# Kernel tuning notes

Hardware: AMD Instinct MI355X
Metric: run time of the kernel (lower is better)

The kernel has to match this reference:

```python
import jax, jax.numpy as jnp
import numpy as np

N_NODES = 100000
N_EDGES = 1600000
NUM_PROP = 5
CAT_PROP = 3
INPUT_DIM = 128
HIDDEN = 128
NUM_REL = 2


def setup_inputs() -> dict:
    key = jax.random.key(0)
    ks = jax.random.split(key, 20)
    s = 0.05
    inp = {
        "x": jax.random.normal(ks[0], (N_NODES, NUM_PROP + CAT_PROP), jnp.float32),
        "edge_index": jax.random.randint(ks[1], (2, N_EDGES), 0, N_NODES, jnp.int64 if jax.config.jax_enable_x64 else jnp.int32),
        "edge_type": jax.random.randint(ks[2], (N_EDGES,), 0, NUM_REL, jnp.int32),
        # numeric / categorical encoders -> input_dim/2 each
        "W_num": jax.random.normal(ks[3], (NUM_PROP, INPUT_DIM // 2), jnp.float32) * s,
        "b_num": jnp.zeros((INPUT_DIM // 2,), jnp.float32),
        "W_cat": jax.random.normal(ks[4], (CAT_PROP, INPUT_DIM // 2), jnp.float32) * s,
        "b_cat": jnp.zeros((INPUT_DIM // 2,), jnp.float32),
        # input projection + PReLU
        "W_in": jax.random.normal(ks[5], (INPUT_DIM, HIDDEN), jnp.float32) * s,
        "b_in": jnp.zeros((HIDDEN,), jnp.float32),
        "prelu_a": jnp.full((HIDDEN,), 0.25, jnp.float32),
        # RGCN layer 1
        "W_rel1": jax.random.normal(ks[6], (NUM_REL, HIDDEN, HIDDEN), jnp.float32) * s,
        "W_root1": jax.random.normal(ks[7], (HIDDEN, HIDDEN), jnp.float32) * s,
        "b_rgcn1": jnp.zeros((HIDDEN,), jnp.float32),
        # RGCN layer 2
        "W_rel2": jax.random.normal(ks[8], (NUM_REL, HIDDEN, HIDDEN), jnp.float32) * s,
        "W_root2": jax.random.normal(ks[9], (HIDDEN, HIDDEN), jnp.float32) * s,
        "b_rgcn2": jnp.zeros((HIDDEN,), jnp.float32),
        # classifier (single Linear)
        "W_cls": jax.random.normal(ks[10], (HIDDEN, HIDDEN), jnp.float32) * s,
        "b_cls": jnp.zeros((HIDDEN,), jnp.float32),
    }
    return inp


def _leaky_relu(x, slope=0.01):
    return jnp.where(x >= 0, x, slope * x)


def _prelu(x, a):
    return jnp.where(x >= 0, x, a * x)


def _rgcn_conv(x, edge_index, edge_type, W_rel, W_root, bias):
    # PyG RGCNConv: out[i] = x[i] @ W_root + bias + sum_r mean_{j in N_r(i)} x[j] @ W_r
    # Aggregate-then-transform (linearity) to avoid per-edge (E, d) @ W products.
    src, dst = edge_index[0], edge_index[1]
    n = x.shape[0]
    x_src = x[src]  # (E, d) gather
    out = x @ W_root + bias
    for r in range(W_rel.shape[0]):
        w = (edge_type == r).astype(x.dtype)  # (E,)
        agg = jax.ops.segment_sum(x_src * w[:, None], dst, num_segments=n)  # (N, d)
        deg = jax.ops.segment_sum(w, dst, num_segments=n)  # (N,)
        out = out + (agg / jnp.clip(deg, 1.0)[:, None]) @ W_rel[r]
    return out


def reference(x, edge_index, edge_type, W_num, b_num, W_cat, b_cat, W_in, b_in,
              prelu_a, W_rel1, W_root1, b_rgcn1, W_rel2, W_root2, b_rgcn2,
              W_cls, b_cls):
    num_prop = x[:, :NUM_PROP]
    cat_prop = x[:, NUM_PROP:NUM_PROP + CAT_PROP]
    n = _leaky_relu(num_prop @ W_num + b_num)
    c = _leaky_relu(cat_prop @ W_cat + b_cat)
    h = jnp.concatenate([n, c], axis=1)
    h = _prelu(h @ W_in + b_in, prelu_a)
    h = _rgcn_conv(h, edge_index, edge_type, W_rel1, W_root1, b_rgcn1)
    # dropout is identity in eval mode
    h = _rgcn_conv(h, edge_index, edge_type, W_rel2, W_root2, b_rgcn2)
    return h @ W_cls + b_cls
```

## Files before the change

### kernel.cpp

```cpp
#include <hip/hip_runtime.h>
#include <cstdint>


typedef short bf16x8 __attribute__((ext_vector_type(8)));
typedef float f32x4  __attribute__((ext_vector_type(4)));

__device__ __forceinline__ unsigned short f2bf(float f) {
    unsigned int u = __builtin_bit_cast(unsigned int, f);
    u += 0x7fff + ((u >> 16) & 1);
    return (unsigned short)(u >> 16);
}
__device__ __forceinline__ float bf2f(unsigned short h) {
    unsigned int u = ((unsigned int)h) << 16;
    return __builtin_bit_cast(float, u);
}
__device__ __forceinline__ float lo16f(unsigned int u) {
    return __builtin_bit_cast(float, u << 16);
}
__device__ __forceinline__ float hi16f(unsigned int u) {
    return __builtin_bit_cast(float, u & 0xffff0000u);
}

__device__ __forceinline__ void gload_lds16(const void* g, void* l) {
    __builtin_amdgcn_global_load_lds(
        (const __attribute__((address_space(1))) void*)g,
        (__attribute__((address_space(3))) void*)l, 16, 0, 0);
}

__global__ __launch_bounds__(256) void k_egemm(
    const float* __restrict__ x,
    const float* __restrict__ Wnum, const float* __restrict__ bnum,
    const float* __restrict__ Wcat, const float* __restrict__ bcat,
    const unsigned short* __restrict__ Bhi, const unsigned short* __restrict__ Blo,
    const float* __restrict__ bias, const float* __restrict__ prelu,
    unsigned short* __restrict__ C_hi, unsigned short* __restrict__ C_lo, int M)
{
    __shared__ unsigned short lds[2][32 * 512];
    const int t = threadIdx.x;
    const int w = t >> 6, lane = t & 63;
    const int laneL = lane & 15, laneH = lane >> 4;
    const int wi = w >> 1, wj = w & 1;
    const int m0 = blockIdx.x * 128;
    const int Mm1 = M - 1;

    f32x4 acc[4][4];
    #pragma unroll
    for (int a = 0; a < 4; ++a)
        #pragma unroll
        for (int b = 0; b < 4; ++b)
            acc[a][b] = (f32x4){0.f, 0.f, 0.f, 0.f};

    auto stage = [&](int s, unsigned short* buf) {
        int koff = s * 32;
        int k8 = koff + laneH * 8;
        #pragma unroll
        for (int c = 0; c < 2; ++c) {
            int j = w + c * 4;
            int rc = j * 16 + laneL;
            int row = (m0 + rc <= Mm1) ? (m0 + rc) : Mm1;
            const float4* xr = (const float4*)(x + (size_t)row * 8);
            float4 X0 = xr[0], X1 = xr[1];
            float a[8];
            if (k8 < 64) {
                const float4* bp = (const float4*)(bnum + k8);
                float4 b0 = bp[0], b1 = bp[1];
                a[0]=b0.x; a[1]=b0.y; a[2]=b0.z; a[3]=b0.w;
                a[4]=b1.x; a[5]=b1.y; a[6]=b1.z; a[7]=b1.w;
                float xs0 = X0.x, xs1 = X0.y, xs2 = X0.z, xs3 = X0.w, xs4 = X1.x;
                const float* wb = Wnum + k8;
                #pragma unroll
                for (int p = 0; p < 5; ++p) {
                    float xp = p==0?xs0 : p==1?xs1 : p==2?xs2 : p==3?xs3 : xs4;
                    const float4* wp = (const float4*)(wb + p * 64);
                    float4 w0 = wp[0], w1 = wp[1];
                    a[0]+=xp*w0.x; a[1]+=xp*w0.y; a[2]+=xp*w0.z; a[3]+=xp*w0.w;
                    a[4]+=xp*w1.x; a[5]+=xp*w1.y; a[6]+=xp*w1.z; a[7]+=xp*w1.w;
                }
            } else {
                int kk = k8 - 64;
                const float4* bp = (const float4*)(bcat + kk);
                float4 b0 = bp[0], b1 = bp[1];
                a[0]=b0.x; a[1]=b0.y; a[2]=b0.z; a[3]=b0.w;
                a[4]=b1.x; a[5]=b1.y; a[6]=b1.z; a[7]=b1.w;
                float xs0 = X1.y, xs1 = X1.z, xs2 = X1.w;
                const float* wb = Wcat + kk;
                #pragma unroll
                for (int p = 0; p < 3; ++p) {
                    float xp = p==0?xs0 : p==1?xs1 : xs2;
                    const float4* wp = (const float4*)(wb + p * 64);
                    float4 w0 = wp[0], w1 = wp[1];
                    a[0]+=xp*w0.x; a[1]+=xp*w0.y; a[2]+=xp*w0.z; a[3]+=xp*w0.w;
                    a[4]+=xp*w1.x; a[5]+=xp*w1.y; a[6]+=xp*w1.z; a[7]+=xp*w1.w;
                }
            }
            unsigned hw[4], lw[4];
            #pragma unroll
            for (int q = 0; q < 4; ++q) {
                float v0 = a[2*q]   >= 0.f ? a[2*q]   : 0.01f * a[2*q];
                float v1 = a[2*q+1] >= 0.f ? a[2*q+1] : 0.01f * a[2*q+1];
                unsigned short h0 = f2bf(v0), h1 = f2bf(v1);
                unsigned short l0 = f2bf(v0 - bf2f(h0)), l1 = f2bf(v1 - bf2f(h1));
                hw[q] = (unsigned)h0 | ((unsigned)h1 << 16);
                lw[q] = (unsigned)l0 | ((unsigned)l1 << 16);
            }
            uint4 ho, lo_;
            ho.x=hw[0]; ho.y=hw[1]; ho.z=hw[2]; ho.w=hw[3];
            lo_.x=lw[0]; lo_.y=lw[1]; lo_.z=lw[2]; lo_.w=lw[3];
            *(uint4*)&buf[(0 * 8 + j) * 512 + lane * 8] = ho;
            *(uint4*)&buf[(1 * 8 + j) * 512 + lane * 8] = lo_;
        }
        #pragma unroll
        for (int c = 4; c < 8; ++c) {
            int chunk = w + c * 4;
            int slot = chunk >> 3, j = chunk & 7;
            const unsigned short* plane = (slot == 2) ? Bhi : Blo;
            int rc = j * 16 + laneL;
            const unsigned short* gp = plane + (size_t)rc * 128 + koff + laneH * 8;
            gload_lds16(gp, &buf[(slot * 8 + j) * 512]);
        }
    };

    stage(0, lds[0]);
    for (int s = 0; s < 4; ++s) {
        unsigned short* cur = lds[s & 1];
        unsigned short* nxt = lds[(s & 1) ^ 1];
        __syncthreads();
        if (s + 1 < 4) stage(s + 1, nxt);
        const bf16x8* fr = (const bf16x8*)cur;
        bf16x8 ah[4], al[4], bh[4], bl[4];
        #pragma unroll
        for (int mi = 0; mi < 4; ++mi) {
            ah[mi] = fr[(0 + wi * 4 + mi) * 64 + lane];
            al[mi] = fr[(8 + wi * 4 + mi) * 64 + lane];
        }
        #pragma unroll
        for (int nj = 0; nj < 4; ++nj) {
            bh[nj] = fr[(16 + wj * 4 + nj) * 64 + lane];
            bl[nj] = fr[(24 + wj * 4 + nj) * 64 + lane];
        }
        #pragma unroll
        for (int mi = 0; mi < 4; ++mi)
            #pragma unroll
            for (int nj = 0; nj < 4; ++nj) {
                acc[mi][nj] = __builtin_amdgcn_mfma_f32_16x16x32_bf16(
                    ah[mi], bh[nj], acc[mi][nj], 0, 0, 0);
                acc[mi][nj] = __builtin_amdgcn_mfma_f32_16x16x32_bf16(
                    ah[mi], bl[nj], acc[mi][nj], 0, 0, 0);
                acc[mi][nj] = __builtin_amdgcn_mfma_f32_16x16x32_bf16(
                    al[mi], bh[nj], acc[mi][nj], 0, 0, 0);
            }
    }

    float bv[4], av[4];
    #pragma unroll
    for (int nj = 0; nj < 4; ++nj) {
        int col = wj * 64 + nj * 16 + laneL;
        bv[nj] = bias[col];
        av[nj] = prelu[col];
    }
    unsigned short* lp = &lds[0][0];
    __syncthreads();
    #pragma unroll
    for (int nj = 0; nj < 4; ++nj) {
        int col = wj * 64 + nj * 16 + laneL;
        #pragma unroll
        for (int mi = 0; mi < 4; ++mi)
            #pragma unroll
            for (int r = 0; r < 4; ++r) {
                int row = wi * 64 + mi * 16 + laneH * 4 + r;
                float v = acc[mi][nj][r] + bv[nj];
                v = v >= 0.f ? v : av[nj] * v;
                lp[row * 128 + col] = f2bf(v);
            }
    }
    __syncthreads();
    {
        const uint4* lsrc = (const uint4*)lp;
        #pragma unroll
        for (int it = 0; it < 8; ++it) {
            int idx = it * 256 + t;
            int row = idx >> 4, c = idx & 15;
            int m = m0 + row;
            if (m < M)
                ((uint4*)(C_hi + (size_t)m * 128))[c] = lsrc[idx];
        }
    }
    __syncthreads();
    #pragma unroll
    for (int nj = 0; nj < 4; ++nj) {
        int col = wj * 64 + nj * 16 + laneL;
        #pragma unroll
        for (int mi = 0; mi < 4; ++mi)
            #pragma unroll
            for (int r = 0; r < 4; ++r) {
                int row = wi * 64 + mi * 16 + laneH * 4 + r;
                float v = acc[mi][nj][r] + bv[nj];
                v = v >= 0.f ? v : av[nj] * v;
                unsigned short h = f2bf(v);
                lp[row * 128 + col] = f2bf(v - bf2f(h));
            }
    }
    __syncthreads();
    {
        const uint4* lsrc = (const uint4*)lp;
        #pragma unroll
        for (int it = 0; it < 8; ++it) {
            int idx = it * 256 + t;
            int row = idx >> 4, c = idx & 15;
            int m = m0 + row;
            if (m < M)
                ((uint4*)(C_lo + (size_t)m * 128))[c] = lsrc[idx];
        }
    }
}

__global__ __launch_bounds__(256) void k_hist(
    const int* __restrict__ ei, const int* __restrict__ et,
    int* __restrict__ cntmatT, int E, int N, int NBINS)
{
    __shared__ int hist[1024];
    const int t = threadIdx.x, blk = blockIdx.x;
    for (int i = t; i < NBINS; i += 256) hist[i] = 0;
    __syncthreads();
    #pragma unroll
    for (int j = 0; j < 8; ++j) {
        int e = blk * 2048 + j * 256 + t;
        if (e < E) atomicAdd(&hist[(et[e] * N + ei[E + e]) >> 8], 1);
    }
    __syncthreads();
    for (int i = t; i < NBINS; i += 256)
        cntmatT[(size_t)blk * NBINS + i] = hist[i];
}

__global__ __launch_bounds__(256) void k_transpose(
    const int* __restrict__ src, int* __restrict__ dst, int R, int C)
{
    __shared__ int tile[32][33];
    int ctiles = (C + 31) >> 5;
    int bx = blockIdx.x % ctiles;
    int by = blockIdx.x / ctiles;
    int tc = threadIdx.x & 31, tr = threadIdx.x >> 5;
    int c0 = bx * 32, r0 = by * 32;
    #pragma unroll
    for (int i = 0; i < 32; i += 8) {
        int r = r0 + tr + i, c = c0 + tc;
        if (r < R && c < C) tile[tr + i][tc] = src[(size_t)r * C + c];
    }
    __syncthreads();
    #pragma unroll
    for (int i = 0; i < 32; i += 8) {
        int r = r0 + tc;
        int c = c0 + tr + i;
        if (r < R && c < C) dst[(size_t)c * R + r] = tile[tc][tr + i];
    }
}

struct WArgs {
    const float* W[8];
    unsigned short* hi[8];
    unsigned short* lo[8];
};
__global__ __launch_bounds__(256) void k_wsplit(WArgs a)
{
    int part = blockIdx.y;
    int idx = blockIdx.x * 256 + threadIdx.x;
    int n = idx >> 7, k = idx & 127;
    float v = a.W[part][(size_t)k * 128 + n];
    unsigned short h = f2bf(v);
    a.hi[part][(size_t)n * 128 + k] = h;
    a.lo[part][(size_t)n * 128 + k] = f2bf(v - bf2f(h));
}

__global__ __launch_bounds__(256) void k_scan1(
    const int* __restrict__ src, int* __restrict__ dst,
    int* __restrict__ bsum, int n)
{
    __shared__ int s[256];
    int t = threadIdx.x;
    int i = blockIdx.x * 256 + t;
    int v = (i < n) ? src[i] : 0;
    s[t] = v;
    __syncthreads();
    #pragma unroll
    for (int d = 1; d < 256; d <<= 1) {
        int add = (t >= d) ? s[t - d] : 0;
        __syncthreads();
        s[t] += add;
        __syncthreads();
    }
    if (i < n) dst[i] = s[t] - v;
    if (t == 255) bsum[blockIdx.x] = s[255];
}

__global__ __launch_bounds__(1024) void k_scan2(int* __restrict__ bsum, int nb)
{
    __shared__ int s[1024];
    int t = threadIdx.x;
    int carry = 0;
    for (int base = 0; base < nb; base += 1024) {
        int i = base + t;
        int v = (i < nb) ? bsum[i] : 0;
        s[t] = v;
        __syncthreads();
        #pragma unroll
        for (int d = 1; d < 1024; d <<= 1) {
            int add = (t >= d) ? s[t - d] : 0;
            __syncthreads();
            s[t] += add;
            __syncthreads();
        }
        if (i < nb) bsum[i] = carry + s[t] - v;
        carry += s[1023];
        __syncthreads();
    }
}

__global__ __launch_bounds__(256) void k_scan3(
    int* __restrict__ dst, const int* __restrict__ bsum, int n)
{
    int i = blockIdx.x * 256 + threadIdx.x;
    if (i < n) dst[i] += bsum[blockIdx.x];
}

__global__ __launch_bounds__(256) void k_binscatter(
    const int* __restrict__ ei, const int* __restrict__ et,
    const int* __restrict__ cntscanT, int* __restrict__ ebuf,
    int E, int N, int NBINS)
{
    __shared__ int base[1024];
    const int t = threadIdx.x;
    const int blk = blockIdx.x;
    for (int i = t; i < NBINS; i += 256)
        base[i] = cntscanT[(size_t)blk * NBINS + i];
    __syncthreads();
    #pragma unroll
    for (int j = 0; j < 8; ++j) {
        int e = blk * 2048 + j * 256 + t;
        if (e < E) {
            unsigned src = (unsigned)ei[e];
            int seg = et[e] * N + ei[E + e];
            int pos = atomicAdd(&base[seg >> 8], 1);
            ebuf[pos] = (int)(((unsigned)(seg & 255) << 24) | src);
        }
    }
}

__global__ __launch_bounds__(256) void k_bincsr(
    const int* __restrict__ cntscan, const int* __restrict__ ebuf,
    int* __restrict__ deg, int* __restrict__ off, int* __restrict__ esrc,
    int E, int nseg, int NBLK, int NBINS)
{
    __shared__ int cnt[256];
    __shared__ int pfx[256];
    __shared__ int cur[256];
    const int b = blockIdx.x;
    const int t = threadIdx.x;
    const int est = cntscan[(size_t)b * NBLK];
    const int een = (b + 1 < NBINS) ? cntscan[(size_t)(b + 1) * NBLK] : E;
    cnt[t] = 0;
    __syncthreads();
    for (int e = est + t; e < een; e += 256)
        atomicAdd(&cnt[((unsigned)ebuf[e]) >> 24], 1);
    __syncthreads();
    int v = cnt[t];
    pfx[t] = v;
    __syncthreads();
    #pragma unroll
    for (int d = 1; d < 256; d <<= 1) {
        int add = (t >= d) ? pfx[t - d] : 0;
        __syncthreads();
        pfx[t] += add;
        __syncthreads();
    }
    int o = est + pfx[t] - v;
    int seg = b * 256 + t;
    if (seg < nseg) { deg[seg] = v; off[seg] = o; }
    cur[t] = o;
    __syncthreads();
    for (int e = est + t; e < een; e += 256) {
        unsigned u = (unsigned)ebuf[e];
        int p = atomicAdd(&cur[u >> 24], 1);
        esrc[p] = (int)(u & 0xffffffu);
    }
}

__global__ __launch_bounds__(256) void k_gather(
    const unsigned short* __restrict__ h_hi,
    const int* __restrict__ esrc,
    const int* __restrict__ off, const int* __restrict__ deg,
    unsigned short* __restrict__ a_hi, int nseg)
{
    int i = blockIdx.x * 8 + (threadIdx.x >> 5);
    if (i >= nseg) return;
    int l32 = threadIdx.x & 31;
    int q = l32 >> 4;
    int l16 = l32 & 15;
    int cnt = deg[i], st = off[i];
    const uint4* hp = (const uint4*)h_hi;
    float a0 = 0.f, a1 = 0.f, a2 = 0.f, a3 = 0.f;
    float a4 = 0.f, a5 = 0.f, a6 = 0.f, a7 = 0.f;
    int e = q;
    for (; e + 6 < cnt; e += 8) {
        int i0 = esrc[st + e + 0];
        int i1 = esrc[st + e + 2];
        int i2 = esrc[st + e + 4];
        int i3 = esrc[st + e + 6];
        uint4 u0 = hp[(size_t)i0 * 16 + l16];
        uint4 u1 = hp[(size_t)i1 * 16 + l16];
        uint4 u2 = hp[(size_t)i2 * 16 + l16];
        uint4 u3 = hp[(size_t)i3 * 16 + l16];
        a0 += lo16f(u0.x); a1 += hi16f(u0.x); a2 += lo16f(u0.y); a3 += hi16f(u0.y);
        a4 += lo16f(u0.z); a5 += hi16f(u0.z); a6 += lo16f(u0.w); a7 += hi16f(u0.w);
        a0 += lo16f(u1.x); a1 += hi16f(u1.x); a2 += lo16f(u1.y); a3 += hi16f(u1.y);
        a4 += lo16f(u1.z); a5 += hi16f(u1.z); a6 += lo16f(u1.w); a7 += hi16f(u1.w);
        a0 += lo16f(u2.x); a1 += hi16f(u2.x); a2 += lo16f(u2.y); a3 += hi16f(u2.y);
        a4 += lo16f(u2.z); a5 += hi16f(u2.z); a6 += lo16f(u2.w); a7 += hi16f(u2.w);
        a0 += lo16f(u3.x); a1 += hi16f(u3.x); a2 += lo16f(u3.y); a3 += hi16f(u3.y);
        a4 += lo16f(u3.z); a5 += hi16f(u3.z); a6 += lo16f(u3.w); a7 += hi16f(u3.w);
    }
    for (; e < cnt; e += 2) {
        uint4 u = hp[(size_t)esrc[st + e] * 16 + l16];
        a0 += lo16f(u.x); a1 += hi16f(u.x); a2 += lo16f(u.y); a3 += hi16f(u.y);
        a4 += lo16f(u.z); a5 += hi16f(u.z); a6 += lo16f(u.w); a7 += hi16f(u.w);
    }
    a0 += __shfl_xor(a0, 16, 64);
    a1 += __shfl_xor(a1, 16, 64);
    a2 += __shfl_xor(a2, 16, 64);
    a3 += __shfl_xor(a3, 16, 64);
    a4 += __shfl_xor(a4, 16, 64);
    a5 += __shfl_xor(a5, 16, 64);
    a6 += __shfl_xor(a6, 16, 64);
    a7 += __shfl_xor(a7, 16, 64);
    if (q == 0) {
        float inv = 1.0f / (float)(cnt > 1 ? cnt : 1);
        uint4 o;
        o.x = (unsigned int)f2bf(a0 * inv) | ((unsigned int)f2bf(a1 * inv) << 16);
        o.y = (unsigned int)f2bf(a2 * inv) | ((unsigned int)f2bf(a3 * inv) << 16);
        o.z = (unsigned int)f2bf(a4 * inv) | ((unsigned int)f2bf(a5 * inv) << 16);
        o.w = (unsigned int)f2bf(a6 * inv) | ((unsigned int)f2bf(a7 * inv) << 16);
        ((uint4*)a_hi)[(size_t)i * 16 + l16] = o;
    }
}

struct GArgs {
    const unsigned short* A_hi[3];
    const unsigned short* A_lo[3];
    const unsigned short* B_hi[3];
    const unsigned short* B_lo[3];
    int alo[3];
    int blo[3];
    const float* bias;
    const float* prelu;
    float* Cf;
    unsigned short* C_hi;
    unsigned short* C_lo;
    int M;
    int P;
};

__global__ __launch_bounds__(256) void k_mgemm(GArgs g)
{
    __shared__ unsigned short lds[2][32 * 512];
    const int t = threadIdx.x;
    const int w = t >> 6, lane = t & 63;
    const int laneL = lane & 15, laneH = lane >> 4;
    const int wi = w >> 1, wj = w & 1;
    const int m0 = blockIdx.x * 128;
    const int Mm1 = g.M - 1;
    const int S = g.P * 4;

    f32x4 acc[4][4];
    #pragma unroll
    for (int a = 0; a < 4; ++a)
        #pragma unroll
        for (int b = 0; b < 4; ++b)
            acc[a][b] = (f32x4){0.f, 0.f, 0.f, 0.f};

    auto stage = [&](int s, unsigned short* buf) {
        int p = s >> 2, koff = (s & 3) * 32;
        const unsigned short* tp[4];
        tp[0] = g.A_hi[p];
        tp[1] = g.alo[p] ? g.A_lo[p] : nullptr;
        tp[2] = g.B_hi[p];
        tp[3] = g.blo[p] ? g.B_lo[p] : nullptr;
        #pragma unroll
        for (int c = 0; c < 8; ++c) {
            int chunk = w + c * 4;
            int slot = chunk >> 3, j = chunk & 7;
            const unsigned short* plane = tp[slot];
            if (!plane) continue;
            int rc = j * 16 + laneL;
            int row = (slot < 2) ? (m0 + rc <= Mm1 ? m0 + rc : Mm1) : rc;
            const unsigned short* gp = plane + (size_t)row * 128 + koff + laneH * 8;
            gload_lds16(gp, &buf[(slot * 8 + j) * 512]);
        }
    };

    stage(0, lds[0]);
    for (int s = 0; s < S; ++s) {
        unsigned short* cur = lds[s & 1];
        unsigned short* nxt = lds[(s & 1) ^ 1];
        __syncthreads();
        if (s + 1 < S) stage(s + 1, nxt);
        int p = s >> 2;
        const bool hasAlo = g.alo[p] != 0;
        const bool hasBlo = g.blo[p] != 0;
        const bf16x8* fr = (const bf16x8*)cur;
        bf16x8 ah[4], al[4], bh[4], bl[4];
        #pragma unroll
        for (int mi = 0; mi < 4; ++mi)
            ah[mi] = fr[(0 + wi * 4 + mi) * 64 + lane];
        if (hasAlo) {
            #pragma unroll
            for (int mi = 0; mi < 4; ++mi)
                al[mi] = fr[(8 + wi * 4 + mi) * 64 + lane];
        }
        #pragma unroll
        for (int nj = 0; nj < 4; ++nj)
            bh[nj] = fr[(16 + wj * 4 + nj) * 64 + lane];
        if (hasBlo) {
            #pragma unroll
            for (int nj = 0; nj < 4; ++nj)
                bl[nj] = fr[(24 + wj * 4 + nj) * 64 + lane];
        }
        #pragma unroll
        for (int mi = 0; mi < 4; ++mi)
            #pragma unroll
            for (int nj = 0; nj < 4; ++nj) {
                acc[mi][nj] = __builtin_amdgcn_mfma_f32_16x16x32_bf16(
                    ah[mi], bh[nj], acc[mi][nj], 0, 0, 0);
                if (hasBlo)
                    acc[mi][nj] = __builtin_amdgcn_mfma_f32_16x16x32_bf16(
                        ah[mi], bl[nj], acc[mi][nj], 0, 0, 0);
                if (hasAlo)
                    acc[mi][nj] = __builtin_amdgcn_mfma_f32_16x16x32_bf16(
                        al[mi], bh[nj], acc[mi][nj], 0, 0, 0);
            }
    }

    const bool hasPrelu = (g.prelu != nullptr);
    float bv[4], av[4];
    #pragma unroll
    for (int nj = 0; nj < 4; ++nj) {
        int col = wj * 64 + nj * 16 + laneL;
        bv[nj] = g.bias[col];
        av[nj] = hasPrelu ? g.prelu[col] : 0.f;
    }

    if (g.Cf) {
        float* lf = (float*)&lds[0][0];
        __syncthreads();
        #pragma unroll
        for (int nj = 0; nj < 4; ++nj) {
            int col = wj * 64 + nj * 16 + laneL;
            #pragma unroll
            for (int mi = 0; mi < 4; ++mi)
                #pragma unroll
                for (int r = 0; r < 4; ++r) {
                    int row = wi * 64 + mi * 16 + laneH * 4 + r;
                    float v = acc[mi][nj][r] + bv[nj];
                    lf[row * 128 + col] = v;
                }
        }
        __syncthreads();
        const uint4* lsrc = (const uint4*)lf;
        #pragma unroll
        for (int it = 0; it < 16; ++it) {
            int idx = it * 256 + t;
            int row = idx >> 5, c = idx & 31;
            int m = m0 + row;
            if (m < g.M)
                ((uint4*)(g.Cf + (size_t)m * 128))[c] = lsrc[idx];
        }
    } else {
        unsigned short* lp = &lds[0][0];
        __syncthreads();
        #pragma unroll
        for (int nj = 0; nj < 4; ++nj) {
            int col = wj * 64 + nj * 16 + laneL;
            #pragma unroll
            for (int mi = 0; mi < 4; ++mi)
                #pragma unroll
                for (int r = 0; r < 4; ++r) {
                    int row = wi * 64 + mi * 16 + laneH * 4 + r;
                    float v = acc[mi][nj][r] + bv[nj];
                    if (hasPrelu) v = v >= 0.f ? v : av[nj] * v;
                    lp[row * 128 + col] = f2bf(v);
                }
        }
        __syncthreads();
        {
            const uint4* lsrc = (const uint4*)lp;
            #pragma unroll
            for (int it = 0; it < 8; ++it) {
                int idx = it * 256 + t;
                int row = idx >> 4, c = idx & 15;
                int m = m0 + row;
                if (m < g.M)
                    ((uint4*)(g.C_hi + (size_t)m * 128))[c] = lsrc[idx];
            }
        }
        __syncthreads();
        #pragma unroll
        for (int nj = 0; nj < 4; ++nj) {
            int col = wj * 64 + nj * 16 + laneL;
            #pragma unroll
            for (int mi = 0; mi < 4; ++mi)
                #pragma unroll
                for (int r = 0; r < 4; ++r) {
                    int row = wi * 64 + mi * 16 + laneH * 4 + r;
                    float v = acc[mi][nj][r] + bv[nj];
                    if (hasPrelu) v = v >= 0.f ? v : av[nj] * v;
                    unsigned short h = f2bf(v);
                    lp[row * 128 + col] = f2bf(v - bf2f(h));
                }
        }
        __syncthreads();
        {
            const uint4* lsrc = (const uint4*)lp;
            #pragma unroll
            for (int it = 0; it < 8; ++it) {
                int idx = it * 256 + t;
                int row = idx >> 4, c = idx & 15;
                int m = m0 + row;
                if (m < g.M)
                    ((uint4*)(g.C_lo + (size_t)m * 128))[c] = lsrc[idx];
            }
        }
    }
}

extern "C" void kernel_launch(void* const* d_in, const int* in_sizes, int n_in,
                              void* d_out, int out_size, void* d_ws, size_t ws_size,
                              hipStream_t stream) {
    const float* x      = (const float*)d_in[0];
    const int*   ei     = (const int*)d_in[1];
    const int*   et     = (const int*)d_in[2];
    const float* Wnum   = (const float*)d_in[3];
    const float* bnum   = (const float*)d_in[4];
    const float* Wcat   = (const float*)d_in[5];
    const float* bcat   = (const float*)d_in[6];
    const float* Win    = (const float*)d_in[7];
    const float* bin    = (const float*)d_in[8];
    const float* pa     = (const float*)d_in[9];
    const float* Wrel1  = (const float*)d_in[10];
    const float* Wroot1 = (const float*)d_in[11];
    const float* brg1   = (const float*)d_in[12];
    const float* Wrel2  = (const float*)d_in[13];
    const float* Wroot2 = (const float*)d_in[14];
    const float* brg2   = (const float*)d_in[15];
    const float* Wcls   = (const float*)d_in[16];
    const float* bcls   = (const float*)d_in[17];
    float* out = (float*)d_out;

    const int N = in_sizes[0] / 8;
    const int E = in_sizes[1] / 2;
    const int nseg = 2 * N;
    const size_t NH = (size_t)N * 128;

    const int NBLK  = (E + 2047) / 2048;
    const int NBINS = (nseg + 255) / 256;
    const long long L = (long long)NBINS * NBLK;

    char* w = (char*)d_ws;
    unsigned short* h0_hi = (unsigned short*)w;  w += NH * 2;
    unsigned short* h0_lo = (unsigned short*)w;  w += NH * 2;
    unsigned short* agg_hi = (unsigned short*)w; w += 2 * NH * 2;
    int* deg      = (int*)w;  w += (size_t)nseg * 4;
    int* off      = (int*)w;  w += (size_t)nseg * 4;
    int* cntmatT  = (int*)w;  w += (size_t)L * 4;
    int* cntmat   = (int*)w;  w += (size_t)L * 4;
    int* cntscan  = (int*)w;  w += (size_t)L * 4;
    int* cntscanT = (int*)w;  w += (size_t)L * 4;
    int* esrc     = (int*)w;  w += (size_t)E * 4;
    int* bsum     = (int*)w;  w += 4096 * 4;
    unsigned short* wplanes = (unsigned short*)w;  w += 8 * 2 * 16384 * 2;

    unsigned short* h1_hi = (unsigned short*)d_out;
    unsigned short* h1_lo = h1_hi + NH;
    unsigned short* h2_hi = h0_hi;
    unsigned short* h2_lo = h0_lo;
    int* ebuf = (int*)d_out;

    unsigned short* whi[8];
    unsigned short* wlo[8];
    for (int i = 0; i < 8; ++i) {
        whi[i] = wplanes + (size_t)i * 2 * 16384;
        wlo[i] = whi[i] + 16384;
    }

    {
        WArgs a;
        a.W[0] = Win;   a.W[1] = Wroot1; a.W[2] = Wrel1; a.W[3] = Wrel1 + 16384;
        a.W[4] = Wroot2; a.W[5] = Wrel2; a.W[6] = Wrel2 + 16384; a.W[7] = Wcls;
        for (int i = 0; i < 8; ++i) { a.hi[i] = whi[i]; a.lo[i] = wlo[i]; }
        k_wsplit<<<dim3(64, 8), 256, 0, stream>>>(a);
    }

    const int gm = (N + 127) / 128;
    const int gg = (nseg + 7) / 8;

    k_hist<<<NBLK, 256, 0, stream>>>(ei, et, cntmatT, E, N, NBINS);

    const int rt = (NBLK + 31) / 32, ct = (NBINS + 31) / 32;
    k_transpose<<<rt * ct, 256, 0, stream>>>(cntmatT, cntmat, NBLK, NBINS);

    const int nb1 = (int)((L + 255) / 256);
    k_scan1<<<nb1, 256, 0, stream>>>(cntmat, cntscan, bsum, (int)L);
    k_scan2<<<1, 1024, 0, stream>>>(bsum, nb1);
    k_scan3<<<nb1, 256, 0, stream>>>(cntscan, bsum, (int)L);

    k_transpose<<<ct * rt, 256, 0, stream>>>(cntscan, cntscanT, NBINS, NBLK);

    k_binscatter<<<NBLK, 256, 0, stream>>>(ei, et, cntscanT, ebuf, E, N, NBINS);
    k_bincsr<<<NBINS, 256, 0, stream>>>(cntscan, ebuf, deg, off, esrc, E, nseg, NBLK, NBINS);

    k_egemm<<<gm, 256, 0, stream>>>(x, Wnum, bnum, Wcat, bcat,
                                    whi[0], wlo[0], bin, pa,
                                    h0_hi, h0_lo, N);

    k_gather<<<gg, 256, 0, stream>>>(h0_hi, esrc, off, deg, agg_hi, nseg);
    {
        GArgs g = {};
        g.A_hi[0] = h0_hi;       g.A_lo[0] = h0_lo;  g.alo[0] = 1; g.blo[0] = 1;
        g.A_hi[1] = agg_hi;      g.alo[1] = 0;       g.blo[1] = 0;
        g.A_hi[2] = agg_hi + NH; g.alo[2] = 0;       g.blo[2] = 0;
        g.B_hi[0] = whi[1]; g.B_lo[0] = wlo[1];
        g.B_hi[1] = whi[2]; g.B_lo[1] = wlo[2];
        g.B_hi[2] = whi[3]; g.B_lo[2] = wlo[3];
        g.bias = brg1; g.prelu = nullptr;
        g.Cf = nullptr; g.C_hi = h1_hi; g.C_lo = h1_lo;
        g.M = N; g.P = 3;
        k_mgemm<<<gm, 256, 0, stream>>>(g);
    }
    k_gather<<<gg, 256, 0, stream>>>(h1_hi, esrc, off, deg, agg_hi, nseg);
    {
        GArgs g = {};
        g.A_hi[0] = h1_hi;       g.A_lo[0] = h1_lo;  g.alo[0] = 1; g.blo[0] = 1;
        g.A_hi[1] = agg_hi;      g.alo[1] = 0;       g.blo[1] = 0;
        g.A_hi[2] = agg_hi + NH; g.alo[2] = 0;       g.blo[2] = 0;
        g.B_hi[0] = whi[4]; g.B_lo[0] = wlo[4];
        g.B_hi[1] = whi[5]; g.B_lo[1] = wlo[5];
        g.B_hi[2] = whi[6]; g.B_lo[2] = wlo[6];
        g.bias = brg2; g.prelu = nullptr;
        g.Cf = nullptr; g.C_hi = h2_hi; g.C_lo = h2_lo;
        g.M = N; g.P = 3;
        k_mgemm<<<gm, 256, 0, stream>>>(g);
    }
    {
        GArgs g = {};
        g.A_hi[0] = h2_hi; g.A_lo[0] = h2_lo; g.alo[0] = 1; g.blo[0] = 1;
        g.B_hi[0] = whi[7]; g.B_lo[0] = wlo[7];
        g.bias = bcls; g.prelu = nullptr;
        g.Cf = out; g.C_hi = nullptr; g.C_lo = nullptr;
        g.M = N; g.P = 1;
        k_mgemm<<<gm, 256, 0, stream>>>(g);
    }
}
```

Baseline: 474.7 us.

## Fuse classifier GEMM into RGCN layer-2 epilogue and merge preprocessing kernels

The classifier linear layer now runs inside the second RGCN GEMM's epilogue. The layer-2 output is split into bf16 hi/lo planes in swizzled LDS and multiplied by the classifier weights there, so the h2 round trip and a separate launch go away. The weight-split and histogram kernels are merged into one launch. The scan-add step is folded into the transpose and into bincsr, and the edge blocks per histogram/scatter block double to 4096. The hi/lo epilogue stores both planes in one pass instead of two. This cuts launches and memory traffic, at the cost of more registers and LDS pressure in the fused epilogue.

```diff
diff --git a/kernel.cpp b/kernel.cpp
--- a/kernel.cpp
+++ b/kernel.cpp
@@ -158,33 +158,8 @@
         bv[nj] = bias[col];
         av[nj] = prelu[col];
     }
-    unsigned short* lp = &lds[0][0];
-    __syncthreads();
-    #pragma unroll
-    for (int nj = 0; nj < 4; ++nj) {
-        int col = wj * 64 + nj * 16 + laneL;
-        #pragma unroll
-        for (int mi = 0; mi < 4; ++mi)
-            #pragma unroll
-            for (int r = 0; r < 4; ++r) {
-                int row = wi * 64 + mi * 16 + laneH * 4 + r;
-                float v = acc[mi][nj][r] + bv[nj];
-                v = v >= 0.f ? v : av[nj] * v;
-                lp[row * 128 + col] = f2bf(v);
-            }
-    }
-    __syncthreads();
-    {
-        const uint4* lsrc = (const uint4*)lp;
-        #pragma unroll
-        for (int it = 0; it < 8; ++it) {
-            int idx = it * 256 + t;
-            int row = idx >> 4, c = idx & 15;
-            int m = m0 + row;
-            if (m < M)
-                ((uint4*)(C_hi + (size_t)m * 128))[c] = lsrc[idx];
-        }
-    }
+    unsigned short* lph = &lds[0][0];
+    unsigned short* lpl = &lds[1][0];
     __syncthreads();
     #pragma unroll
     for (int nj = 0; nj < 4; ++nj) {
@@ -197,39 +172,64 @@
                 float v = acc[mi][nj][r] + bv[nj];
                 v = v >= 0.f ? v : av[nj] * v;
                 unsigned short h = f2bf(v);
-                lp[row * 128 + col] = f2bf(v - bf2f(h));
+                lph[row * 128 + col] = h;
+                lpl[row * 128 + col] = f2bf(v - bf2f(h));
             }
     }
     __syncthreads();
     {
-        const uint4* lsrc = (const uint4*)lp;
+        const uint4* sh = (const uint4*)lph;
+        const uint4* sl = (const uint4*)lpl;
         #pragma unroll
         for (int it = 0; it < 8; ++it) {
             int idx = it * 256 + t;
             int row = idx >> 4, c = idx & 15;
             int m = m0 + row;
-            if (m < M)
-                ((uint4*)(C_lo + (size_t)m * 128))[c] = lsrc[idx];
-        }
-    }
-}
-
-__global__ __launch_bounds__(256) void k_hist(
-    const int* __restrict__ ei, const int* __restrict__ et,
-    int* __restrict__ cntmatT, int E, int N, int NBINS)
+            if (m < M) {
+                ((uint4*)(C_hi + (size_t)m * 128))[c] = sh[idx];
+                ((uint4*)(C_lo + (size_t)m * 128))[c] = sl[idx];
+            }
+        }
+    }
+}
+
+struct WHArgs {
+    const float* W[8];
+    unsigned short* hi[8];
+    unsigned short* lo[8];
+    const int* ei;
+    const int* et;
+    int* cntmatT;
+    int E;
+    int N;
+    int NBINS;
+};
+__global__ __launch_bounds__(256) void k_wsplit_hist(WHArgs a)
 {
     __shared__ int hist[1024];
-    const int t = threadIdx.x, blk = blockIdx.x;
-    for (int i = t; i < NBINS; i += 256) hist[i] = 0;
-    __syncthreads();
-    #pragma unroll
-    for (int j = 0; j < 8; ++j) {
-        int e = blk * 2048 + j * 256 + t;
-        if (e < E) atomicAdd(&hist[(et[e] * N + ei[E + e]) >> 8], 1);
-    }
-    __syncthreads();
-    for (int i = t; i < NBINS; i += 256)
-        cntmatT[(size_t)blk * NBINS + i] = hist[i];
+    const int t = threadIdx.x;
+    const int b = blockIdx.x;
+    if (b < 512) {
+        int part = b >> 6;
+        int idx = (b & 63) * 256 + t;
+        int n = idx >> 7, k = idx & 127;
+        float v = a.W[part][(size_t)k * 128 + n];
+        unsigned short h = f2bf(v);
+        a.hi[part][(size_t)n * 128 + k] = h;
+        a.lo[part][(size_t)n * 128 + k] = f2bf(v - bf2f(h));
+        return;
+    }
+    const int blk = b - 512;
+    for (int i = t; i < a.NBINS; i += 256) hist[i] = 0;
+    __syncthreads();
+    #pragma unroll
+    for (int j = 0; j < 16; ++j) {
+        int e = blk * 4096 + j * 256 + t;
+        if (e < a.E) atomicAdd(&hist[(a.et[e] * a.N + a.ei[a.E + e]) >> 8], 1);
+    }
+    __syncthreads();
+    for (int i = t; i < a.NBINS; i += 256)
+        a.cntmatT[(size_t)blk * a.NBINS + i] = hist[i];
 }
 
 __global__ __launch_bounds__(256) void k_transpose(
@@ -255,20 +255,31 @@
     }
 }
 
-struct WArgs {
-    const float* W[8];
-    unsigned short* hi[8];
-    unsigned short* lo[8];
-};
-__global__ __launch_bounds__(256) void k_wsplit(WArgs a)
-{
-    int part = blockIdx.y;
-    int idx = blockIdx.x * 256 + threadIdx.x;
-    int n = idx >> 7, k = idx & 127;
-    float v = a.W[part][(size_t)k * 128 + n];
-    unsigned short h = f2bf(v);
-    a.hi[part][(size_t)n * 128 + k] = h;
-    a.lo[part][(size_t)n * 128 + k] = f2bf(v - bf2f(h));
+__global__ __launch_bounds__(256) void k_transpose_add(
+    const int* __restrict__ src, int* __restrict__ dst,
+    const int* __restrict__ bsum, int R, int C)
+{
+    __shared__ int tile[32][33];
+    int ctiles = (C + 31) >> 5;
+    int bx = blockIdx.x % ctiles;
+    int by = blockIdx.x / ctiles;
+    int tc = threadIdx.x & 31, tr = threadIdx.x >> 5;
+    int c0 = bx * 32, r0 = by * 32;
+    #pragma unroll
+    for (int i = 0; i < 32; i += 8) {
+        int r = r0 + tr + i, c = c0 + tc;
+        if (r < R && c < C) {
+            size_t idx = (size_t)r * C + c;
+            tile[tr + i][tc] = src[idx] + bsum[idx >> 8];
+        }
+    }
+    __syncthreads();
+    #pragma unroll
+    for (int i = 0; i < 32; i += 8) {
+        int r = r0 + tc;
+        int c = c0 + tr + i;
+        if (r < R && c < C) dst[(size_t)c * R + r] = tile[tc][tr + i];
+    }
 }
 
 __global__ __launch_bounds__(256) void k_scan1(
@@ -315,13 +326,6 @@
     }
 }
 
-__global__ __launch_bounds__(256) void k_scan3(
-    int* __restrict__ dst, const int* __restrict__ bsum, int n)
-{
-    int i = blockIdx.x * 256 + threadIdx.x;
-    if (i < n) dst[i] += bsum[blockIdx.x];
-}
-
 __global__ __launch_bounds__(256) void k_binscatter(
     const int* __restrict__ ei, const int* __restrict__ et,
     const int* __restrict__ cntscanT, int* __restrict__ ebuf,
@@ -334,8 +338,8 @@
         base[i] = cntscanT[(size_t)blk * NBINS + i];
     __syncthreads();
     #pragma unroll
-    for (int j = 0; j < 8; ++j) {
-        int e = blk * 2048 + j * 256 + t;
+    for (int j = 0; j < 16; ++j) {
+        int e = blk * 4096 + j * 256 + t;
         if (e < E) {
             unsigned src = (unsigned)ei[e];
             int seg = et[e] * N + ei[E + e];
@@ -346,7 +350,8 @@
 }
 
 __global__ __launch_bounds__(256) void k_bincsr(
-    const int* __restrict__ cntscan, const int* __restrict__ ebuf,
+    const int* __restrict__ cntscan, const int* __restrict__ bsum,
+    const int* __restrict__ ebuf,
     int* __restrict__ deg, int* __restrict__ off, int* __restrict__ esrc,
     int E, int nseg, int NBLK, int NBINS)
 {
@@ -355,8 +360,13 @@
     __shared__ int cur[256];
     const int b = blockIdx.x;
     const int t = threadIdx.x;
-    const int est = cntscan[(size_t)b * NBLK];
-    const int een = (b + 1 < NBINS) ? cntscan[(size_t)(b + 1) * NBLK] : E;
+    size_t i0 = (size_t)b * NBLK;
+    const int est = cntscan[i0] + bsum[i0 >> 8];
+    int een = E;
+    if (b + 1 < NBINS) {
+        size_t i1 = (size_t)(b + 1) * NBLK;
+        een = cntscan[i1] + bsum[i1 >> 8];
+    }
     cnt[t] = 0;
     __syncthreads();
     for (int e = est + t; e < een; e += 256)
@@ -451,11 +461,14 @@
     int blo[3];
     const float* bias;
     const float* prelu;
-    float* Cf;
     unsigned short* C_hi;
     unsigned short* C_lo;
     int M;
     int P;
+    const unsigned short* clsBhi;
+    const unsigned short* clsBlo;
+    const float* clsBias;
+    float* outF;
 };
 
 __global__ __launch_bounds__(256) void k_mgemm(GArgs g)
@@ -538,17 +551,14 @@
             }
     }
 
-    const bool hasPrelu = (g.prelu != nullptr);
-    float bv[4], av[4];
-    #pragma unroll
-    for (int nj = 0; nj < 4; ++nj) {
-        int col = wj * 64 + nj * 16 + laneL;
-        bv[nj] = g.bias[col];
-        av[nj] = hasPrelu ? g.prelu[col] : 0.f;
-    }
-
-    if (g.Cf) {
-        float* lf = (float*)&lds[0][0];
+    float bv[4];
+    #pragma unroll
+    for (int nj = 0; nj < 4; ++nj)
+        bv[nj] = g.bias[wj * 64 + nj * 16 + laneL];
+
+    if (g.clsBhi) {
+        char* l0 = (char*)&lds[0][0];
+        char* l1 = (char*)&lds[1][0];
         __syncthreads();
         #pragma unroll
         for (int nj = 0; nj < 4; ++nj) {
@@ -559,7 +569,63 @@
                 for (int r = 0; r < 4; ++r) {
                     int row = wi * 64 + mi * 16 + laneH * 4 + r;
                     float v = acc[mi][nj][r] + bv[nj];
-                    lf[row * 128 + col] = v;
+                    unsigned short h = f2bf(v);
+                    int offb = row * 256 + ((col * 2) ^ ((row & 7) << 4));
+                    *(unsigned short*)(l0 + offb) = h;
+                    *(unsigned short*)(l1 + offb) = f2bf(v - bf2f(h));
+                }
+        }
+        __syncthreads();
+        f32x4 acc2[4][4];
+        #pragma unroll
+        for (int a = 0; a < 4; ++a)
+            #pragma unroll
+            for (int b = 0; b < 4; ++b)
+                acc2[a][b] = (f32x4){0.f, 0.f, 0.f, 0.f};
+        #pragma unroll
+        for (int ks = 0; ks < 4; ++ks) {
+            bf16x8 ah2[4], al2[4], bh2[4], bl2[4];
+            #pragma unroll
+            for (int mi = 0; mi < 4; ++mi) {
+                int rc = wi * 64 + mi * 16 + laneL;
+                int aoff = rc * 256 + ((ks * 64 + laneH * 16) ^ ((rc & 7) << 4));
+                ah2[mi] = *(const bf16x8*)(l0 + aoff);
+                al2[mi] = *(const bf16x8*)(l1 + aoff);
+            }
+            #pragma unroll
+            for (int nj = 0; nj < 4; ++nj) {
+                int rc = wj * 64 + nj * 16 + laneL;
+                size_t boff = (size_t)rc * 128 + ks * 32 + laneH * 8;
+                bh2[nj] = *(const bf16x8*)(g.clsBhi + boff);
+                bl2[nj] = *(const bf16x8*)(g.clsBlo + boff);
+            }
+            #pragma unroll
+            for (int mi = 0; mi < 4; ++mi)
+                #pragma unroll
+                for (int nj = 0; nj < 4; ++nj) {
+                    acc2[mi][nj] = __builtin_amdgcn_mfma_f32_16x16x32_bf16(
+                        ah2[mi], bh2[nj], acc2[mi][nj], 0, 0, 0);
+                    acc2[mi][nj] = __builtin_amdgcn_mfma_f32_16x16x32_bf16(
+                        ah2[mi], bl2[nj], acc2[mi][nj], 0, 0, 0);
+                    acc2[mi][nj] = __builtin_amdgcn_mfma_f32_16x16x32_bf16(
+                        al2[mi], bh2[nj], acc2[mi][nj], 0, 0, 0);
+                }
+        }
+        float cb[4];
+        #pragma unroll
+        for (int nj = 0; nj < 4; ++nj)
+            cb[nj] = g.clsBias[wj * 64 + nj * 16 + laneL];
+        float* lf = (float*)&lds[0][0];
+        __syncthreads();
+        #pragma unroll
+        for (int nj = 0; nj < 4; ++nj) {
+            int col = wj * 64 + nj * 16 + laneL;
+            #pragma unroll
+            for (int mi = 0; mi < 4; ++mi)
+                #pragma unroll
+                for (int r = 0; r < 4; ++r) {
+                    int row = wi * 64 + mi * 16 + laneH * 4 + r;
+                    lf[row * 128 + col] = acc2[mi][nj][r] + cb[nj];
                 }
         }
         __syncthreads();
@@ -570,61 +636,47 @@
             int row = idx >> 5, c = idx & 31;
             int m = m0 + row;
             if (m < g.M)
-                ((uint4*)(g.Cf + (size_t)m * 128))[c] = lsrc[idx];
-        }
-    } else {
-        unsigned short* lp = &lds[0][0];
-        __syncthreads();
-        #pragma unroll
-        for (int nj = 0; nj < 4; ++nj) {
-            int col = wj * 64 + nj * 16 + laneL;
-            #pragma unroll
-            for (int mi = 0; mi < 4; ++mi)
-                #pragma unroll
-                for (int r = 0; r < 4; ++r) {
-                    int row = wi * 64 + mi * 16 + laneH * 4 + r;
-                    float v = acc[mi][nj][r] + bv[nj];
-                    if (hasPrelu) v = v >= 0.f ? v : av[nj] * v;
-                    lp[row * 128 + col] = f2bf(v);
-                }
-        }
-        __syncthreads();
-        {
-            const uint4* lsrc = (const uint4*)lp;
-            #pragma unroll
-            for (int it = 0; it < 8; ++it) {
-                int idx = it * 256 + t;
-                int row = idx >> 4, c = idx & 15;
-                int m = m0 + row;
-                if (m < g.M)
-                    ((uint4*)(g.C_hi + (size_t)m * 128))[c] = lsrc[idx];
-            }
-        }
-        __syncthreads();
-        #pragma unroll
-        for (int nj = 0; nj < 4; ++nj) {
-            int col = wj * 64 + nj * 16 + laneL;
-            #pragma unroll
-            for (int mi = 0; mi < 4; ++mi)
-                #pragma unroll
-                for (int r = 0; r < 4; ++r) {
-                    int row = wi * 64 + mi * 16 + laneH * 4 + r;
-                    float v = acc[mi][nj][r] + bv[nj];
-                    if (hasPrelu) v = v >= 0.f ? v : av[nj] * v;
-                    unsigned short h = f2bf(v);
-                    lp[row * 128 + col] = f2bf(v - bf2f(h));
-                }
-        }
-        __syncthreads();
-        {
-            const uint4* lsrc = (const uint4*)lp;
-            #pragma unroll
-            for (int it = 0; it < 8; ++it) {
-                int idx = it * 256 + t;
-                int row = idx >> 4, c = idx & 15;
-                int m = m0 + row;
-                if (m < g.M)
-                    ((uint4*)(g.C_lo + (size_t)m * 128))[c] = lsrc[idx];
+                ((uint4*)(g.outF + (size_t)m * 128))[c] = lsrc[idx];
+        }
+        return;
+    }
+
+    const bool hasPrelu = (g.prelu != nullptr);
+    float av[4];
+    #pragma unroll
+    for (int nj = 0; nj < 4; ++nj)
+        av[nj] = hasPrelu ? g.prelu[wj * 64 + nj * 16 + laneL] : 0.f;
+
+    unsigned short* lph = &lds[0][0];
+    unsigned short* lpl = &lds[1][0];
+    __syncthreads();
+    #pragma unroll
+    for (int nj = 0; nj < 4; ++nj) {
+        int col = wj * 64 + nj * 16 + laneL;
+        #pragma unroll
+        for (int mi = 0; mi < 4; ++mi)
+            #pragma unroll
+            for (int r = 0; r < 4; ++r) {
+                int row = wi * 64 + mi * 16 + laneH * 4 + r;
+                float v = acc[mi][nj][r] + bv[nj];
+                if (hasPrelu) v = v >= 0.f ? v : av[nj] * v;
+                unsigned short h = f2bf(v);
+                lph[row * 128 + col] = h;
+                lpl[row * 128 + col] = f2bf(v - bf2f(h));
+            }
+    }
+    __syncthreads();
+    {
+        const uint4* sh = (const uint4*)lph;
+        const uint4* sl = (const uint4*)lpl;
+        #pragma unroll
+        for (int it = 0; it < 8; ++it) {
+            int idx = it * 256 + t;
+            int row = idx >> 4, c = idx & 15;
+            int m = m0 + row;
+            if (m < g.M) {
+                ((uint4*)(g.C_hi + (size_t)m * 128))[c] = sh[idx];
+                ((uint4*)(g.C_lo + (size_t)m * 128))[c] = sl[idx];
             }
         }
     }
@@ -658,13 +710,13 @@
     const int nseg = 2 * N;
     const size_t NH = (size_t)N * 128;
 
-    const int NBLK  = (E + 2047) / 2048;
+    const int NBLK  = (E + 4095) / 4096;
     const int NBINS = (nseg + 255) / 256;
     const long long L = (long long)NBINS * NBLK;
 
     char* w = (char*)d_ws;
-    unsigned short* h0_hi = (unsigned short*)w;  w += NH * 2;
-    unsigned short* h0_lo = (unsigned short*)w;  w += NH * 2;
+    unsigned short* h1_hi = (unsigned short*)w;  w += NH * 2;
+    unsigned short* h1_lo = (unsigned short*)w;  w += NH * 2;
     unsigned short* agg_hi = (unsigned short*)w; w += 2 * NH * 2;
     int* deg      = (int*)w;  w += (size_t)nseg * 4;
     int* off      = (int*)w;  w += (size_t)nseg * 4;
@@ -676,11 +728,9 @@
     int* bsum     = (int*)w;  w += 4096 * 4;
     unsigned short* wplanes = (unsigned short*)w;  w += 8 * 2 * 16384 * 2;
 
-    unsigned short* h1_hi = (unsigned short*)d_out;
-    unsigned short* h1_lo = h1_hi + NH;
-    unsigned short* h2_hi = h0_hi;
-    unsigned short* h2_lo = h0_lo;
     int* ebuf = (int*)d_out;
+    unsigned short* h0_hi = (unsigned short*)d_out;
+    unsigned short* h0_lo = h0_hi + NH;
 
     unsigned short* whi[8];
     unsigned short* wlo[8];
@@ -689,31 +739,31 @@
         wlo[i] = whi[i] + 16384;
     }
 
+    const int gm = (N + 127) / 128;
+    const int gg = (nseg + 7) / 8;
+
     {
-        WArgs a;
+        WHArgs a;
         a.W[0] = Win;   a.W[1] = Wroot1; a.W[2] = Wrel1; a.W[3] = Wrel1 + 16384;
         a.W[4] = Wroot2; a.W[5] = Wrel2; a.W[6] = Wrel2 + 16384; a.W[7] = Wcls;
         for (int i = 0; i < 8; ++i) { a.hi[i] = whi[i]; a.lo[i] = wlo[i]; }
-        k_wsplit<<<dim3(64, 8), 256, 0, stream>>>(a);
-    }
-
-    const int gm = (N + 127) / 128;
-    const int gg = (nseg + 7) / 8;
-
-    k_hist<<<NBLK, 256, 0, stream>>>(ei, et, cntmatT, E, N, NBINS);
-
-    const int rt = (NBLK + 31) / 32, ct = (NBINS + 31) / 32;
-    k_transpose<<<rt * ct, 256, 0, stream>>>(cntmatT, cntmat, NBLK, NBINS);
+        a.ei = ei; a.et = et; a.cntmatT = cntmatT;
+        a.E = E; a.N = N; a.NBINS = NBINS;
+        k_wsplit_hist<<<512 + NBLK, 256, 0, stream>>>(a);
+    }
+
+    k_transpose<<<((NBLK + 31) / 32) * ((NBINS + 31) / 32), 256, 0, stream>>>(
+        cntmatT, cntmat, NBLK, NBINS);
 
     const int nb1 = (int)((L + 255) / 256);
     k_scan1<<<nb1, 256, 0, stream>>>(cntmat, cntscan, bsum, (int)L);
     k_scan2<<<1, 1024, 0, stream>>>(bsum, nb1);
-    k_scan3<<<nb1, 256, 0, stream>>>(cntscan, bsum, (int)L);
-
-    k_transpose<<<ct * rt, 256, 0, stream>>>(cntscan, cntscanT, NBINS, NBLK);
+    k_transpose_add<<<((NBINS + 31) / 32) * ((NBLK + 31) / 32), 256, 0, stream>>>(
+        cntscan, cntscanT, bsum, NBINS, NBLK);
 
     k_binscatter<<<NBLK, 256, 0, stream>>>(ei, et, cntscanT, ebuf, E, N, NBINS);
-    k_bincsr<<<NBINS, 256, 0, stream>>>(cntscan, ebuf, deg, off, esrc, E, nseg, NBLK, NBINS);
+    k_bincsr<<<NBINS, 256, 0, stream>>>(cntscan, bsum, ebuf, deg, off, esrc,
+                                        E, nseg, NBLK, NBINS);
 
     k_egemm<<<gm, 256, 0, stream>>>(x, Wnum, bnum, Wcat, bcat,
                                     whi[0], wlo[0], bin, pa,
@@ -729,8 +779,9 @@
         g.B_hi[1] = whi[2]; g.B_lo[1] = wlo[2];
         g.B_hi[2] = whi[3]; g.B_lo[2] = wlo[3];
         g.bias = brg1; g.prelu = nullptr;
-        g.Cf = nullptr; g.C_hi = h1_hi; g.C_lo = h1_lo;
+        g.C_hi = h1_hi; g.C_lo = h1_lo;
         g.M = N; g.P = 3;
+        g.clsBhi = nullptr;
         k_mgemm<<<gm, 256, 0, stream>>>(g);
     }
     k_gather<<<gg, 256, 0, stream>>>(h1_hi, esrc, off, deg, agg_hi, nseg);
@@ -743,17 +794,10 @@
         g.B_hi[1] = whi[5]; g.B_lo[1] = wlo[5];
         g.B_hi[2] = whi[6]; g.B_lo[2] = wlo[6];
         g.bias = brg2; g.prelu = nullptr;
-        g.Cf = nullptr; g.C_hi = h2_hi; g.C_lo = h2_lo;
+        g.C_hi = nullptr; g.C_lo = nullptr;
         g.M = N; g.P = 3;
+        g.clsBhi = whi[7]; g.clsBlo = wlo[7];
+        g.clsBias = bcls; g.outF = out;
         k_mgemm<<<gm, 256, 0, stream>>>(g);
     }
-    {
-        GArgs g = {};
-        g.A_hi[0] = h2_hi; g.A_lo[0] = h2_lo; g.alo[0] = 1; g.blo[0] = 1;
-        g.B_hi[0] = whi[7]; g.B_lo[0] = wlo[7];
-        g.bias = bcls; g.prelu = nullptr;
-        g.Cf = out; g.C_hi = nullptr; g.C_lo = nullptr;
-        g.M = N; g.P = 1;
-        k_mgemm<<<gm, 256, 0, stream>>>(g);
-    }
-}
+}
```

Result: faster. 436.3 us (median of 2 runs) (-8.1%).
